# Optimization experiments

Hardware: AMD Instinct MI355X
Metric: run time of the kernel (lower is better)

The kernel has to match this reference:

```python
import math
import jax, jax.numpy as jnp
import numpy as np

NH, D, MULT, VOCAB, NLAYER = 4, 256, 128, 256, 2
N = MULT * D // NH  # 8192
EPS = 1e-5
THETA = 2.0 ** 16


def get_freqs(n):
    q = (jnp.arange(n, dtype=jnp.float32) // 2) * 2  # quantize(t, 2)
    return 1.0 / (THETA ** (q / n)) / (2 * math.pi)


def ln(x):
    # LayerNorm over last dim, no affine
    mu = jnp.mean(x, axis=-1, keepdims=True)
    var = jnp.mean((x - mu) ** 2, axis=-1, keepdims=True)
    return (x - mu) / jnp.sqrt(var + EPS)


def rope(phases, v):
    # phases: (T, N), v: (B, nh, T, N)
    ph = (phases % 1.0) * (2 * math.pi)
    c, s = jnp.cos(ph), jnp.sin(ph)
    v_rot = jnp.stack((-v[..., 1::2], v[..., ::2]), axis=-1).reshape(v.shape)
    return v * c + v_rot * s


def setup_inputs() -> dict:
    key = jax.random.key(0)
    ks = jax.random.split(key, 6)
    std = 0.02
    return {
        "idx": jax.random.randint(ks[0], (1, 2048), 0, VOCAB),
        "embed": jax.random.normal(ks[1], (VOCAB, D), jnp.float32) * std,
        "encoder": jax.random.normal(ks[2], (NH, D, N), jnp.float32) * std,
        "encoder_v": jax.random.normal(ks[3], (NH, D, N), jnp.float32) * std,
        "decoder": jax.random.normal(ks[4], (NH * N, D), jnp.float32) * std,
        "lm_head": jax.random.normal(ks[5], (D, VOCAB), jnp.float32) * std,
    }


def reference(idx, embed, encoder, encoder_v, decoder, lm_head):
    B, T = idx.shape
    freqs = get_freqs(N)  # (N,)
    phases = jnp.arange(T, dtype=jnp.float32)[:, None] * freqs[None, :]  # (T, N)
    # strictly-lower-triangular causal mask (tril diagonal=-1)
    t = jnp.arange(T)
    mask = (t[:, None] > t[None, :]).astype(jnp.float32)  # (T, T)

    x = ln(embed[idx][:, None])  # (B, 1, T, D)
    for _ in range(NLAYER):
        x_sparse = jax.nn.relu(jnp.einsum('bltd,hdn->bhtn', x, encoder))  # (B,nh,T,N)
        QR = rope(phases, x_sparse)
        scores = jnp.einsum('bhtn,bhsn->bhts', QR, QR) * mask  # (B,nh,T,T)
        yKV = ln(jnp.einsum('bhts,blsd->bhtd', scores, x))  # (B,nh,T,D)
        y_sparse = jax.nn.relu(jnp.einsum('bhtd,hdn->bhtn', yKV, encoder_v))
        xy = x_sparse * y_sparse  # (B,nh,T,N)
        xy = xy.transpose(0, 2, 1, 3).reshape(B, 1, T, NH * N)
        yMLP = xy @ decoder  # (B,1,T,D)
        x = ln(x + ln(yMLP))
    logits = x[:, 0] @ lm_head  # (B,T,vocab)
    return logits
```

## Files before the change

### kernel.cpp

```cpp
#include <hip/hip_runtime.h>
#include <hip/hip_bf16.h>
#include <math.h>

typedef unsigned short u16;
typedef unsigned int u32;
typedef __attribute__((ext_vector_type(8))) short short8;
typedef __attribute__((ext_vector_type(4))) float f32x4;

__device__ __forceinline__ u16 f2b(float f) {
  u32 u = __builtin_bit_cast(u32, f);
  u = (u + 0x7fffu + ((u >> 16) & 1u)) >> 16;
  return (u16)u;
}
__device__ __forceinline__ float b2f(u16 s) {
  return __builtin_bit_cast(float, (u32)s << 16);
}

__device__ __forceinline__ void ld_g2l(const u16* g, u16* l) {
  __builtin_amdgcn_global_load_lds(
      (const __attribute__((address_space(1))) unsigned int*)g,
      (__attribute__((address_space(3))) unsigned int*)l, 16, 0, 0);
}

__device__ __forceinline__ void gemm_core(
    const u16* __restrict__ A, const u16* __restrict__ B,
    int lda, int ldb, int Klen, int kb, int bm, int bn,
    u16* __restrict__ As, u16* __restrict__ Bs, f32x4 (&acc)[4][4])
{
  int tid = threadIdx.x;
  int w = tid >> 6, lane = tid & 63;
  int srow = (w << 4) + (lane >> 2);
  int scol = (lane & 3) << 3;
  const u16* ga0 = A + (long)(bm * 128 + srow) * lda + kb + scol;
  const u16* ga1 = ga0 + (long)64 * lda;
  const u16* gb0 = B + (long)(bn * 128 + srow) * ldb + kb + scol;
  const u16* gb1 = gb0 + (long)64 * ldb;
  u16* la0 = As + (w << 9);  u16* la1 = la0 + 2048;
  u16* lb0 = Bs + (w << 9);  u16* lb1 = lb0 + 2048;

  int wm = (w >> 1) << 6, wn = (w & 1) << 6;
  int lane15 = lane & 15, quad = lane >> 4;
  const u16* ar = As + (wm + lane15) * 32 + quad * 8;
  const u16* br = Bs + (wn + lane15) * 32 + quad * 8;

#pragma unroll
  for (int i = 0; i < 4; i++)
#pragma unroll
    for (int j = 0; j < 4; j++) { f32x4 z = {0.f, 0.f, 0.f, 0.f}; acc[i][j] = z; }

  for (int k = 0; k < Klen; k += 32) {
    ld_g2l(ga0 + k, la0);
    ld_g2l(ga1 + k, la1);
    ld_g2l(gb0 + k, lb0);
    ld_g2l(gb1 + k, lb1);
    __syncthreads();
    short8 af[4], bfr[4];
#pragma unroll
    for (int mt = 0; mt < 4; mt++) af[mt] = *(const short8*)(ar + mt * 16 * 32);
#pragma unroll
    for (int nt = 0; nt < 4; nt++) bfr[nt] = *(const short8*)(br + nt * 16 * 32);
#pragma unroll
    for (int mt = 0; mt < 4; mt++)
#pragma unroll
      for (int nt = 0; nt < 4; nt++)
        acc[mt][nt] = __builtin_amdgcn_mfma_f32_16x16x32_bf16(af[mt], bfr[nt], acc[mt][nt], 0, 0, 0);
    __syncthreads();
  }
}

__device__ __forceinline__ void rope_cs(int n, int t, float& c, float& s) {
  float f = exp2f((float)(-(n & ~1)) * (1.0f / 512.0f)) * 0.15915494f;
  float ph = (float)t * f;
  ph -= floorf(ph);
  __sincosf(ph * 6.2831853f, &s, &c);
}

template<int EPI>
__global__ __launch_bounds__(256, 2) void gemm_bt(
    const u16* __restrict__ A, const u16* __restrict__ B, void* __restrict__ C,
    int K, int lda, int ldb, int ldc, int nsplits, long aB, long bB, long cB,
    int tri)
{
  __shared__ __align__(16) u16 As[128 * 32];
  __shared__ __align__(16) u16 Bs[128 * 32];
  int bn = blockIdx.x, bm = blockIdx.y;
  int batch = blockIdx.z / nsplits, sp = blockIdx.z % nsplits;
  int Klen = K / nsplits, kb = sp * Klen;
  if (tri) {
    int kend = (bm + 1) * 128;
    if (kb >= kend) return;
    if (kb + Klen > kend) Klen = kend - kb;
  }

  f32x4 acc[4][4];
  gemm_core(A + (long)batch * aB, B + (long)batch * bB, lda, ldb, Klen, kb, bm, bn, As, Bs, acc);

  int lane = threadIdx.x & 63, w = threadIdx.x >> 6;
  int wm = (w >> 1) << 6, wn = (w & 1) << 6;
  int lane15 = lane & 15, quad = lane >> 4;

#pragma unroll
  for (int mt = 0; mt < 4; mt++)
#pragma unroll
    for (int nt = 0; nt < 4; nt++) {
      int gn = bn * 128 + wn + nt * 16 + lane15;
#pragma unroll
      for (int r = 0; r < 4; r++) {
        int gm = bm * 128 + wm + mt * 16 + quad * 4 + r;
        float v = acc[mt][nt][r];
        long ci = (long)batch * cB + (long)gm * ldc + gn;
        if (EPI == 0) {
          ((float*)C)[ci] = v;
        } else if (EPI == 1) {
          float rv = fmaxf(v, 0.f);
          float ro = __shfl_xor(rv, 1);
          float c, s; rope_cs(gn, gm, c, s);
          float out = (gn & 1) ? (rv * c + ro * s) : (rv * c - ro * s);
          ((u16*)C)[ci] = f2b(out);
        } else if (EPI == 3) {
          atomicAdd(&((float*)C)[ci], v);
        } else if (EPI == 4) {
          u16* Cp = (u16*)C;
          float q = b2f(Cp[ci]);
          float qo = __shfl_xor(q, 1);
          float c, s; rope_cs(gn, gm, c, s);
          float xs = (gn & 1) ? (q * c - qo * s) : (q * c + qo * s);
          Cp[ci] = f2b(fmaxf(v, 0.f) * xs);
        }
      }
    }
}

#define SC_BAR   __builtin_amdgcn_s_barrier()
#define SC_LGKM0 asm volatile("s_waitcnt lgkmcnt(0)" ::: "memory")
#define SC_LGKM8 asm volatile("s_waitcnt lgkmcnt(8)" ::: "memory")
#define SC_VMF   do { asm volatile("s_waitcnt vmcnt(4)" ::: "memory"); \
                      __builtin_amdgcn_sched_barrier(0); } while (0)
#define SC_P1    __builtin_amdgcn_s_setprio(1)
#define SC_P0    __builtin_amdgcn_s_setprio(0)

#define DSA(Ab, mh) { \
  _Pragma("unroll") for (int mt = 0; mt < 4; mt++) { \
    aA[mt][0] = *(const short8*)((Ab) + ((mh) * 64 + mt * 16) * 64 + koff0); \
    aA[mt][1] = *(const short8*)((Ab) + ((mh) * 64 + mt * 16) * 64 + koff1); } }

#define DSB(Bb, nh, dst) { \
  _Pragma("unroll") for (int nt = 0; nt < 2; nt++) { \
    dst[nt][0] = *(const short8*)((Bb) + ((nh) * 32 + nt * 16) * 64 + koff0); \
    dst[nt][1] = *(const short8*)((Bb) + ((nh) * 32 + nt * 16) * 64 + koff1); } }

#define MMA(MH, NH, BB) { \
  _Pragma("unroll") for (int mt = 0; mt < 4; mt++) \
  _Pragma("unroll") for (int nt = 0; nt < 2; nt++) { \
    acc[(MH)*4+mt][(NH)*2+nt] = __builtin_amdgcn_mfma_f32_16x16x32_bf16( \
        aA[mt][0], BB[nt][0], acc[(MH)*4+mt][(NH)*2+nt], 0, 0, 0); \
    acc[(MH)*4+mt][(NH)*2+nt] = __builtin_amdgcn_mfma_f32_16x16x32_bf16( \
        aA[mt][1], BB[nt][1], acc[(MH)*4+mt][(NH)*2+nt], 0, 0, 0); } }

__global__ __launch_bounds__(512, 1) void gemm_scores8(
    const u16* __restrict__ QR, u16* __restrict__ S, int T)
{
  __shared__ __align__(16) u16 Abuf[2][256 * 64];
  __shared__ __align__(16) u16 Bbuf[2][256 * 64];

  int q = blockIdx.x;
  int bm = (int)((sqrtf(8.f * (float)q + 1.f) - 1.f) * 0.5f);
  while ((bm + 1) * (bm + 2) / 2 <= q) bm++;
  while (bm * (bm + 1) / 2 > q) bm--;
  int bn = q - bm * (bm + 1) / 2;

  const u16* Q = QR + (long)blockIdx.z * (long)T * 8192;
  u16* Sb = S + (long)blockIdx.z * (long)T * T;

  int tid = threadIdx.x;
  int w = tid >> 6, lane = tid & 63;
  int wr = w >> 2, wc = w & 3;
  int lane15 = lane & 15, quad = lane >> 4;
  int swz = lane15 & 7;
  int koff0 = ((quad) ^ swz) << 3;
  int koff1 = ((4 + quad) ^ swz) << 3;

  const u16* gA = Q + (long)(bm * 256) * 8192;
  const u16* gB = Q + (long)(bn * 256) * 8192;

  const u16* A0 = &Abuf[0][(wr * 128 + lane15) * 64];
  const u16* A1 = &Abuf[1][(wr * 128 + lane15) * 64];
  const u16* B0 = &Bbuf[0][(wc * 64 + lane15) * 64];
  const u16* B1 = &Bbuf[1][(wc * 64 + lane15) * 64];

  int sr = lane >> 3, sc = lane & 7;
  long g_sk = (long)sr * 8192 + ((sc ^ sr) << 3);
  int l_base = (w * 16) * 64;
  long g_wrow = (long)(w * 16) * 8192;

  auto STG = [&](const u16* gHalfBase, u16* lHalfBase, int kt) {
    const u16* g = gHalfBase + g_wrow + g_sk + kt * 64;
    u16* l = lHalfBase + l_base;
    ld_g2l(g, l);
    ld_g2l(g + (long)8 * 8192, l + 8 * 64);
  };

  f32x4 acc[8][4];
#pragma unroll
  for (int i2 = 0; i2 < 8; i2++)
#pragma unroll
    for (int j = 0; j < 4; j++) { f32x4 z = {0.f, 0.f, 0.f, 0.f}; acc[i2][j] = z; }

  const long HSTEP = (long)128 * 8192;

  STG(gA, &Abuf[0][0], 0); STG(gA + HSTEP, &Abuf[0][128 * 64], 0);
  STG(gB, &Bbuf[0][0], 0); STG(gB + HSTEP, &Bbuf[0][128 * 64], 0);
  STG(gB, &Bbuf[1][0], 1); STG(gB + HSTEP, &Bbuf[1][128 * 64], 1);
  SC_VMF;
  SC_BAR;

  const int nkt = 8192 / 64;
  for (int i = 0; i < nkt / 2; i++) {
    int kt1 = 2 * i + 1;
    int kt2 = 2 * i + 2; if (kt2 > nkt - 1) kt2 = nkt - 1;
    int kt3 = 2 * i + 3; if (kt3 > nkt - 1) kt3 = nkt - 1;
    short8 aA[4][2], bb0[2][2], bb1[2][2];

    DSA(A0, 0); DSB(B0, 0, bb0);
    STG(gA, &Abuf[1][0], kt1);
    SC_LGKM8; SC_BAR; SC_LGKM0; SC_P1; MMA(0, 0, bb0); SC_P0; SC_BAR;
    DSB(B0, 1, bb1);
    STG(gA + HSTEP, &Abuf[1][128 * 64], kt1);
    SC_BAR; SC_LGKM0; SC_P1; MMA(0, 1, bb1); SC_P0; SC_BAR;
    DSA(A0, 1);
    STG(gB, &Bbuf[0][0], kt2);
    SC_BAR; SC_LGKM0; SC_P1; MMA(1, 1, bb1); SC_P0; SC_BAR;
    STG(gB + HSTEP, &Bbuf[0][128 * 64], kt2);
    SC_VMF; SC_BAR; SC_LGKM0; SC_P1; MMA(1, 0, bb0); SC_P0; SC_BAR;

    DSA(A1, 0); DSB(B1, 0, bb0);
    STG(gA, &Abuf[0][0], kt2);
    SC_LGKM8; SC_BAR; SC_LGKM0; SC_P1; MMA(0, 0, bb0); SC_P0; SC_BAR;
    DSB(B1, 1, bb1);
    STG(gA + HSTEP, &Abuf[0][128 * 64], kt2);
    SC_BAR; SC_LGKM0; SC_P1; MMA(0, 1, bb1); SC_P0; SC_BAR;
    DSA(A1, 1);
    STG(gB, &Bbuf[1][0], kt3);
    SC_BAR; SC_LGKM0; SC_P1; MMA(1, 1, bb1); SC_P0; SC_BAR;
    STG(gB + HSTEP, &Bbuf[1][128 * 64], kt3);
    SC_VMF; SC_BAR; SC_LGKM0; SC_P1; MMA(1, 0, bb0); SC_P0; SC_BAR;
  }

#pragma unroll
  for (int mt = 0; mt < 8; mt++)
#pragma unroll
    for (int nt = 0; nt < 4; nt++) {
      int gn = bn * 256 + wc * 64 + nt * 16 + lane15;
#pragma unroll
      for (int r = 0; r < 4; r++) {
        int gm = bm * 256 + wr * 128 + mt * 16 + quad * 4 + r;
        Sb[(long)gm * T + gn] = f2b(gm > gn ? acc[mt][nt][r] : 0.f);
      }
    }
}

__global__ __launch_bounds__(256) void trans_f32_bf16(
    const float* __restrict__ src, u16* __restrict__ dst, int R, int C)
{
  __shared__ float tile[32][33];
  long off = (long)blockIdx.z * R * C;
  const float* s = src + off;
  u16* d = dst + off;
  int lx = threadIdx.x & 31, ly = threadIdx.x >> 5;
  int c = blockIdx.x * 32 + lx;
#pragma unroll
  for (int p = 0; p < 32; p += 8)
    tile[ly + p][lx] = s[(long)(blockIdx.y * 32 + ly + p) * C + c];
  __syncthreads();
  int rr = blockIdx.y * 32 + lx;
#pragma unroll
  for (int p = 0; p < 32; p += 8)
    d[(long)(blockIdx.x * 32 + ly + p) * R + rr] = f2b(tile[lx][ly + p]);
}

__device__ __forceinline__ float block_sum(float v, float* red) {
#pragma unroll
  for (int o = 32; o > 0; o >>= 1) v += __shfl_down(v, o, 64);
  int lane = threadIdx.x & 63, wid = threadIdx.x >> 6;
  if (lane == 0) red[wid] = v;
  __syncthreads();
  float r = red[0] + red[1] + red[2] + red[3];
  __syncthreads();
  return r;
}

__global__ __launch_bounds__(256) void embed_ln(
    const int* __restrict__ idx, const float* __restrict__ embed,
    float* __restrict__ x, u16* __restrict__ xb, u16* __restrict__ xT, int T)
{
  __shared__ float red[4];
  int t = blockIdx.x, d = threadIdx.x;
  float v = embed[(long)idx[t] * 256 + d];
  float mu = block_sum(v, red) * (1.f / 256.f);
  float c = v - mu;
  float var = block_sum(c * c, red) * (1.f / 256.f);
  float o = c * rsqrtf(var + 1e-5f);
  x[(long)t * 256 + d] = o;
  xb[(long)t * 256 + d] = f2b(o);
  xT[(long)d * T + t] = f2b(o);
}

__global__ __launch_bounds__(256) void row_ln(
    const float* __restrict__ in, u16* __restrict__ out)
{
  __shared__ float red[4];
  long row = blockIdx.x;
  int d = threadIdx.x;
  float v = in[row * 256 + d];
  float mu = block_sum(v, red) * (1.f / 256.f);
  float c = v - mu;
  float var = block_sum(c * c, red) * (1.f / 256.f);
  out[row * 256 + d] = f2b(c * rsqrtf(var + 1e-5f));
}

__global__ __launch_bounds__(256) void resid_ln(
    const float* __restrict__ yMLP, float* __restrict__ x,
    u16* __restrict__ xb, u16* __restrict__ xT, int T)
{
  __shared__ float red[4];
  int t = blockIdx.x, d = threadIdx.x;
  float y = yMLP[(long)t * 256 + d];
  float mu1 = block_sum(y, red) * (1.f / 256.f);
  float c1 = y - mu1;
  float var1 = block_sum(c1 * c1, red) * (1.f / 256.f);
  float l1 = c1 * rsqrtf(var1 + 1e-5f);
  float v = x[(long)t * 256 + d] + l1;
  float mu2 = block_sum(v, red) * (1.f / 256.f);
  float c2 = v - mu2;
  float var2 = block_sum(c2 * c2, red) * (1.f / 256.f);
  float o = c2 * rsqrtf(var2 + 1e-5f);
  x[(long)t * 256 + d] = o;
  xb[(long)t * 256 + d] = f2b(o);
  xT[(long)d * T + t] = f2b(o);
}

extern "C" void kernel_launch(void* const* d_in, const int* in_sizes, int n_in,
                              void* d_out, int out_size, void* d_ws, size_t ws_size,
                              hipStream_t stream) {
  const int*   idx       = (const int*)d_in[0];
  const float* embed     = (const float*)d_in[1];
  const float* encoder   = (const float*)d_in[2];
  const float* encoder_v = (const float*)d_in[3];
  const float* decoder   = (const float*)d_in[4];
  const float* lm_head   = (const float*)d_in[5];
  const int T = in_sizes[0];
  const int D = 256, NH = 4, Nn = 8192, V = 256;

  char* ws = (char*)d_ws;
  size_t off = 0;
  auto alloc = [&](size_t bytes) -> void* {
    void* p = ws + off; off += (bytes + 255) & ~(size_t)255; return p;
  };
  float* x_f32   = (float*)alloc((size_t)T * D * 4);
  float* yMLP    = (float*)alloc((size_t)T * D * 4);
  float* yKV_f32 = (float*)alloc((size_t)NH * T * D * 4);
  u16* x_b    = (u16*)alloc((size_t)T * D * 2);
  u16* xT     = (u16*)alloc((size_t)T * D * 2);
  u16* yKV_b  = (u16*)alloc((size_t)NH * T * D * 2);
  u16* lmT    = (u16*)alloc((size_t)D * V * 2);
  u16* encT   = (u16*)alloc((size_t)NH * Nn * D * 2);
  u16* encvT  = (u16*)alloc((size_t)NH * Nn * D * 2);
  u16* decT   = (u16*)alloc((size_t)D * NH * Nn * 2);
  size_t per_head = ((size_t)T * T * 2 + 256) + ((size_t)T * Nn * 2 + 256);
  int HB = 4;
  while (HB > 1 && off + (size_t)HB * per_head > ws_size) HB >>= 1;
  u16* scores = (u16*)alloc((size_t)HB * T * T * 2);
  u16* QRxy   = (u16*)alloc((size_t)HB * T * Nn * 2);
  if (off > ws_size) return;

  trans_f32_bf16<<<dim3(Nn / 32, D / 32, NH), 256, 0, stream>>>(encoder, encT, D, Nn);
  trans_f32_bf16<<<dim3(Nn / 32, D / 32, NH), 256, 0, stream>>>(encoder_v, encvT, D, Nn);
  trans_f32_bf16<<<dim3(D / 32, (NH * Nn) / 32, 1), 256, 0, stream>>>(decoder, decT, NH * Nn, D);
  trans_f32_bf16<<<dim3(V / 32, D / 32, 1), 256, 0, stream>>>(lm_head, lmT, D, V);

  embed_ln<<<T, 256, 0, stream>>>(idx, embed, x_f32, x_b, xT, T);

  const int nbm = T / 256, ntri = nbm * (nbm + 1) / 2;

  for (int l = 0; l < 2; l++) {
    hipMemsetAsync(yMLP, 0, (size_t)T * D * 4, stream);
    for (int h0 = 0; h0 < NH; h0 += HB) {
      gemm_bt<1><<<dim3(Nn / 128, T / 128, HB), 256, 0, stream>>>(
          x_b, encT + (size_t)h0 * Nn * D, QRxy,
          D, D, D, Nn, 1, 0L, (long)Nn * D, (long)T * Nn, 0);
      gemm_scores8<<<dim3(ntri, 1, HB), 512, 0, stream>>>(QRxy, scores, T);
      hipMemsetAsync(yKV_f32, 0, (size_t)HB * T * D * 4, stream);
      gemm_bt<3><<<dim3(D / 128, T / 128, HB * 8), 256, 0, stream>>>(
          scores, xT, yKV_f32,
          T, T, T, D, 8, (long)T * T, 0L, (long)T * D, 1);
      row_ln<<<HB * T, 256, 0, stream>>>(yKV_f32, yKV_b);
      gemm_bt<4><<<dim3(Nn / 128, T / 128, HB), 256, 0, stream>>>(
          yKV_b, encvT + (size_t)h0 * Nn * D, QRxy,
          D, D, D, Nn, 1, (long)T * D, (long)Nn * D, (long)T * Nn, 0);
      gemm_bt<3><<<dim3(D / 128, T / 128, HB * 8), 256, 0, stream>>>(
          QRxy, decT + (size_t)h0 * Nn, yMLP,
          Nn, Nn, NH * Nn, D, 8, (long)T * Nn, (long)Nn, 0L, 0);
    }
    resid_ln<<<T, 256, 0, stream>>>(yMLP, x_f32, x_b, xT, T);
  }

  gemm_bt<0><<<dim3(V / 128, T / 128, 1), 256, 0, stream>>>(
      x_b, lmT, d_out, D, D, D, V, 1, 0L, 0L, 0L, 0);
}
```

Measured before the change: 1.214 ms.

## Generalize 256x256 eight-phase pipelined GEMM and use it for encoder and decoder GEMMs

Factors the eight-phase double-buffered 512-thread 256x256 MFMA loop from the scores kernel into a macro. It adds a templated general GEMM with the RoPE, relu-product and atomic epilogues. The encoder, encoder_v and decoder GEMMs switch from 128x128 256-thread tiles to this kernel, aiming for more reuse per block and better overlap of loads with MFMA. Grids shrink sharply (e.g. the decoder GEMM has only 1 N-tile), which risks lower occupancy or poor SM fill. K=256 also gives only 4 k-tiles, so the pipeline's prologue and epilogue dominate.

```diff
diff --git a/kernel.cpp b/kernel.cpp
--- a/kernel.cpp
+++ b/kernel.cpp
@@ -111,7 +111,227 @@
         long ci = (long)batch * cB + (long)gm * ldc + gn;
         if (EPI == 0) {
           ((float*)C)[ci] = v;
-        } else if (EPI == 1) {
+        } else if (EPI == 3) {
+          atomicAdd(&((float*)C)[ci], v);
+        }
+      }
+    }
+}
+
+#define SC_BAR   __builtin_amdgcn_s_barrier()
+#define SC_LGKM0 asm volatile("s_waitcnt lgkmcnt(0)" ::: "memory")
+#define SC_LGKM8 asm volatile("s_waitcnt lgkmcnt(8)" ::: "memory")
+#define SC_VMF   do { asm volatile("s_waitcnt vmcnt(4)" ::: "memory"); \
+                      __builtin_amdgcn_sched_barrier(0); } while (0)
+#define SC_P1    __builtin_amdgcn_s_setprio(1)
+#define SC_P0    __builtin_amdgcn_s_setprio(0)
+
+#define DSA(Ab, mh) { \
+  _Pragma("unroll") for (int mt = 0; mt < 4; mt++) { \
+    aA[mt][0] = *(const short8*)((Ab) + ((mh) * 64 + mt * 16) * 64 + koff0); \
+    aA[mt][1] = *(const short8*)((Ab) + ((mh) * 64 + mt * 16) * 64 + koff1); } }
+
+#define DSB(Bb, nh, dst) { \
+  _Pragma("unroll") for (int nt = 0; nt < 2; nt++) { \
+    dst[nt][0] = *(const short8*)((Bb) + ((nh) * 32 + nt * 16) * 64 + koff0); \
+    dst[nt][1] = *(const short8*)((Bb) + ((nh) * 32 + nt * 16) * 64 + koff1); } }
+
+#define MMA(MH, NH, BB) { \
+  _Pragma("unroll") for (int mt = 0; mt < 4; mt++) \
+  _Pragma("unroll") for (int nt = 0; nt < 2; nt++) { \
+    acc[(MH)*4+mt][(NH)*2+nt] = __builtin_amdgcn_mfma_f32_16x16x32_bf16( \
+        aA[mt][0], BB[nt][0], acc[(MH)*4+mt][(NH)*2+nt], 0, 0, 0); \
+    acc[(MH)*4+mt][(NH)*2+nt] = __builtin_amdgcn_mfma_f32_16x16x32_bf16( \
+        aA[mt][1], BB[nt][1], acc[(MH)*4+mt][(NH)*2+nt], 0, 0, 0); } }
+
+#define EIGHT_PHASE_LOOP(STGA, STGB) \
+  for (int i = 0; i < nkt / 2; i++) { \
+    int kt1 = 2 * i + 1; \
+    int kt2 = 2 * i + 2; if (kt2 > nkt - 1) kt2 = nkt - 1; \
+    int kt3 = 2 * i + 3; if (kt3 > nkt - 1) kt3 = nkt - 1; \
+    short8 aA[4][2], bb0[2][2], bb1[2][2]; \
+     \
+    DSA(A0, 0); DSB(B0, 0, bb0); \
+    STGA(gA, &Abuf[1][0], kt1); \
+    SC_LGKM8; SC_BAR; SC_LGKM0; SC_P1; MMA(0, 0, bb0); SC_P0; SC_BAR; \
+     \
+    DSB(B0, 1, bb1); \
+    STGA(gA + HSTEPA, &Abuf[1][128 * 64], kt1); \
+    SC_BAR; SC_LGKM0; SC_P1; MMA(0, 1, bb1); SC_P0; SC_BAR; \
+     \
+    DSA(A0, 1); \
+    STGB(gB, &Bbuf[0][0], kt2); \
+    SC_BAR; SC_LGKM0; SC_P1; MMA(1, 1, bb1); SC_P0; SC_BAR; \
+     \
+    STGB(gB + HSTEPB, &Bbuf[0][128 * 64], kt2); \
+    SC_VMF; SC_BAR; SC_LGKM0; SC_P1; MMA(1, 0, bb0); SC_P0; SC_BAR; \
+     \
+    DSA(A1, 0); DSB(B1, 0, bb0); \
+    STGA(gA, &Abuf[0][0], kt2); \
+    SC_LGKM8; SC_BAR; SC_LGKM0; SC_P1; MMA(0, 0, bb0); SC_P0; SC_BAR; \
+     \
+    DSB(B1, 1, bb1); \
+    STGA(gA + HSTEPA, &Abuf[0][128 * 64], kt2); \
+    SC_BAR; SC_LGKM0; SC_P1; MMA(0, 1, bb1); SC_P0; SC_BAR; \
+     \
+    DSA(A1, 1); \
+    STGB(gB, &Bbuf[1][0], kt3); \
+    SC_BAR; SC_LGKM0; SC_P1; MMA(1, 1, bb1); SC_P0; SC_BAR; \
+     \
+    STGB(gB + HSTEPB, &Bbuf[1][128 * 64], kt3); \
+    SC_VMF; SC_BAR; SC_LGKM0; SC_P1; MMA(1, 0, bb0); SC_P0; SC_BAR; \
+  }
+
+__global__ __launch_bounds__(512, 1) void gemm_scores8(
+    const u16* __restrict__ QR, u16* __restrict__ S, int T)
+{
+  __shared__ __align__(16) u16 Abuf[2][256 * 64];
+  __shared__ __align__(16) u16 Bbuf[2][256 * 64];
+
+  int q = blockIdx.x;
+  int bm = (int)((sqrtf(8.f * (float)q + 1.f) - 1.f) * 0.5f);
+  while ((bm + 1) * (bm + 2) / 2 <= q) bm++;
+  while (bm * (bm + 1) / 2 > q) bm--;
+  int bn = q - bm * (bm + 1) / 2;
+
+  const u16* Q = QR + (long)blockIdx.z * (long)T * 8192;
+  u16* Sb = S + (long)blockIdx.z * (long)T * T;
+
+  int tid = threadIdx.x;
+  int w = tid >> 6, lane = tid & 63;
+  int wr = w >> 2, wc = w & 3;
+  int lane15 = lane & 15, quad = lane >> 4;
+  int swz = lane15 & 7;
+  int koff0 = ((quad) ^ swz) << 3;
+  int koff1 = ((4 + quad) ^ swz) << 3;
+
+  const u16* gA = Q + (long)(bm * 256) * 8192;
+  const u16* gB = Q + (long)(bn * 256) * 8192;
+
+  const u16* A0 = &Abuf[0][(wr * 128 + lane15) * 64];
+  const u16* A1 = &Abuf[1][(wr * 128 + lane15) * 64];
+  const u16* B0 = &Bbuf[0][(wc * 64 + lane15) * 64];
+  const u16* B1 = &Bbuf[1][(wc * 64 + lane15) * 64];
+
+  int sr = lane >> 3, sc = lane & 7;
+  long g_sk = (long)sr * 8192 + ((sc ^ sr) << 3);
+  int l_base = (w * 16) * 64;
+  long g_wrow = (long)(w * 16) * 8192;
+
+  auto STG = [&](const u16* gHalfBase, u16* lHalfBase, int kt) {
+    const u16* g = gHalfBase + g_wrow + g_sk + kt * 64;
+    u16* l = lHalfBase + l_base;
+    ld_g2l(g, l);
+    ld_g2l(g + (long)8 * 8192, l + 8 * 64);
+  };
+
+  f32x4 acc[8][4];
+#pragma unroll
+  for (int i2 = 0; i2 < 8; i2++)
+#pragma unroll
+    for (int j = 0; j < 4; j++) { f32x4 z = {0.f, 0.f, 0.f, 0.f}; acc[i2][j] = z; }
+
+  const long HSTEPA = (long)128 * 8192;
+  const long HSTEPB = HSTEPA;
+
+  STG(gA, &Abuf[0][0], 0); STG(gA + HSTEPA, &Abuf[0][128 * 64], 0);
+  STG(gB, &Bbuf[0][0], 0); STG(gB + HSTEPB, &Bbuf[0][128 * 64], 0);
+  STG(gB, &Bbuf[1][0], 1); STG(gB + HSTEPB, &Bbuf[1][128 * 64], 1);
+  SC_VMF;
+  SC_BAR;
+
+  const int nkt = 8192 / 64;
+  EIGHT_PHASE_LOOP(STG, STG)
+
+#pragma unroll
+  for (int mt = 0; mt < 8; mt++)
+#pragma unroll
+    for (int nt = 0; nt < 4; nt++) {
+      int gn = bn * 256 + wc * 64 + nt * 16 + lane15;
+#pragma unroll
+      for (int r = 0; r < 4; r++) {
+        int gm = bm * 256 + wr * 128 + mt * 16 + quad * 4 + r;
+        Sb[(long)gm * T + gn] = f2b(gm > gn ? acc[mt][nt][r] : 0.f);
+      }
+    }
+}
+
+template<int EPI>
+__global__ __launch_bounds__(512, 1) void gemm256_8ph(
+    const u16* __restrict__ A, const u16* __restrict__ B, void* __restrict__ C,
+    int K, int lda, int ldb, int ldc, int nsplits, long aB, long bB, long cB)
+{
+  __shared__ __align__(16) u16 Abuf[2][256 * 64];
+  __shared__ __align__(16) u16 Bbuf[2][256 * 64];
+
+  int bn = blockIdx.x, bm = blockIdx.y;
+  int batch = blockIdx.z / nsplits, sp = blockIdx.z % nsplits;
+  int Klen = K / nsplits, kb = sp * Klen;
+  int nkt = Klen >> 6;
+
+  int tid = threadIdx.x;
+  int w = tid >> 6, lane = tid & 63;
+  int wr = w >> 2, wc = w & 3;
+  int lane15 = lane & 15, quad = lane >> 4;
+  int swz = lane15 & 7;
+  int koff0 = ((quad) ^ swz) << 3;
+  int koff1 = ((4 + quad) ^ swz) << 3;
+
+  const u16* gA = A + (long)batch * aB + (long)(bm * 256) * lda + kb;
+  const u16* gB = B + (long)batch * bB + (long)(bn * 256) * ldb + kb;
+
+  const u16* A0 = &Abuf[0][(wr * 128 + lane15) * 64];
+  const u16* A1 = &Abuf[1][(wr * 128 + lane15) * 64];
+  const u16* B0 = &Bbuf[0][(wc * 64 + lane15) * 64];
+  const u16* B1 = &Bbuf[1][(wc * 64 + lane15) * 64];
+
+  int sr = lane >> 3, sc = lane & 7;
+  int l_base = (w * 16) * 64;
+  long g_skA = (long)sr * lda + ((sc ^ sr) << 3);
+  long g_skB = (long)sr * ldb + ((sc ^ sr) << 3);
+  long g_wrowA = (long)(w * 16) * lda;
+  long g_wrowB = (long)(w * 16) * ldb;
+  const long HSTEPA = (long)128 * lda;
+  const long HSTEPB = (long)128 * ldb;
+
+  auto STGA = [&](const u16* gHalfBase, u16* lHalfBase, int kt) {
+    const u16* g = gHalfBase + g_wrowA + g_skA + kt * 64;
+    u16* l = lHalfBase + l_base;
+    ld_g2l(g, l);
+    ld_g2l(g + (long)8 * lda, l + 8 * 64);
+  };
+  auto STGB = [&](const u16* gHalfBase, u16* lHalfBase, int kt) {
+    const u16* g = gHalfBase + g_wrowB + g_skB + kt * 64;
+    u16* l = lHalfBase + l_base;
+    ld_g2l(g, l);
+    ld_g2l(g + (long)8 * ldb, l + 8 * 64);
+  };
+
+  f32x4 acc[8][4];
+#pragma unroll
+  for (int i2 = 0; i2 < 8; i2++)
+#pragma unroll
+    for (int j = 0; j < 4; j++) { f32x4 z = {0.f, 0.f, 0.f, 0.f}; acc[i2][j] = z; }
+
+  STGA(gA, &Abuf[0][0], 0); STGA(gA + HSTEPA, &Abuf[0][128 * 64], 0);
+  STGB(gB, &Bbuf[0][0], 0); STGB(gB + HSTEPB, &Bbuf[0][128 * 64], 0);
+  STGB(gB, &Bbuf[1][0], 1); STGB(gB + HSTEPB, &Bbuf[1][128 * 64], 1);
+  SC_VMF;
+  SC_BAR;
+
+  EIGHT_PHASE_LOOP(STGA, STGB)
+
+#pragma unroll
+  for (int mt = 0; mt < 8; mt++)
+#pragma unroll
+    for (int nt = 0; nt < 4; nt++) {
+      int gn = bn * 256 + wc * 64 + nt * 16 + lane15;
+#pragma unroll
+      for (int r = 0; r < 4; r++) {
+        int gm = bm * 256 + wr * 128 + mt * 16 + quad * 4 + r;
+        float v = acc[mt][nt][r];
+        long ci = (long)batch * cB + (long)gm * ldc + gn;
+        if (EPI == 1) {
           float rv = fmaxf(v, 0.f);
           float ro = __shfl_xor(rv, 1);
           float c, s; rope_cs(gn, gm, c, s);
@@ -121,140 +341,12 @@
           atomicAdd(&((float*)C)[ci], v);
         } else if (EPI == 4) {
           u16* Cp = (u16*)C;
-          float q = b2f(Cp[ci]);
-          float qo = __shfl_xor(q, 1);
+          float qv = b2f(Cp[ci]);
+          float qo = __shfl_xor(qv, 1);
           float c, s; rope_cs(gn, gm, c, s);
-          float xs = (gn & 1) ? (q * c - qo * s) : (q * c + qo * s);
+          float xs = (gn & 1) ? (qv * c - qo * s) : (qv * c + qo * s);
           Cp[ci] = f2b(fmaxf(v, 0.f) * xs);
         }
-      }
-    }
-}
-
-#define SC_BAR   __builtin_amdgcn_s_barrier()
-#define SC_LGKM0 asm volatile("s_waitcnt lgkmcnt(0)" ::: "memory")
-#define SC_LGKM8 asm volatile("s_waitcnt lgkmcnt(8)" ::: "memory")
-#define SC_VMF   do { asm volatile("s_waitcnt vmcnt(4)" ::: "memory"); \
-                      __builtin_amdgcn_sched_barrier(0); } while (0)
-#define SC_P1    __builtin_amdgcn_s_setprio(1)
-#define SC_P0    __builtin_amdgcn_s_setprio(0)
-
-#define DSA(Ab, mh) { \
-  _Pragma("unroll") for (int mt = 0; mt < 4; mt++) { \
-    aA[mt][0] = *(const short8*)((Ab) + ((mh) * 64 + mt * 16) * 64 + koff0); \
-    aA[mt][1] = *(const short8*)((Ab) + ((mh) * 64 + mt * 16) * 64 + koff1); } }
-
-#define DSB(Bb, nh, dst) { \
-  _Pragma("unroll") for (int nt = 0; nt < 2; nt++) { \
-    dst[nt][0] = *(const short8*)((Bb) + ((nh) * 32 + nt * 16) * 64 + koff0); \
-    dst[nt][1] = *(const short8*)((Bb) + ((nh) * 32 + nt * 16) * 64 + koff1); } }
-
-#define MMA(MH, NH, BB) { \
-  _Pragma("unroll") for (int mt = 0; mt < 4; mt++) \
-  _Pragma("unroll") for (int nt = 0; nt < 2; nt++) { \
-    acc[(MH)*4+mt][(NH)*2+nt] = __builtin_amdgcn_mfma_f32_16x16x32_bf16( \
-        aA[mt][0], BB[nt][0], acc[(MH)*4+mt][(NH)*2+nt], 0, 0, 0); \
-    acc[(MH)*4+mt][(NH)*2+nt] = __builtin_amdgcn_mfma_f32_16x16x32_bf16( \
-        aA[mt][1], BB[nt][1], acc[(MH)*4+mt][(NH)*2+nt], 0, 0, 0); } }
-
-__global__ __launch_bounds__(512, 1) void gemm_scores8(
-    const u16* __restrict__ QR, u16* __restrict__ S, int T)
-{
-  __shared__ __align__(16) u16 Abuf[2][256 * 64];
-  __shared__ __align__(16) u16 Bbuf[2][256 * 64];
-
-  int q = blockIdx.x;
-  int bm = (int)((sqrtf(8.f * (float)q + 1.f) - 1.f) * 0.5f);
-  while ((bm + 1) * (bm + 2) / 2 <= q) bm++;
-  while (bm * (bm + 1) / 2 > q) bm--;
-  int bn = q - bm * (bm + 1) / 2;
-
-  const u16* Q = QR + (long)blockIdx.z * (long)T * 8192;
-  u16* Sb = S + (long)blockIdx.z * (long)T * T;
-
-  int tid = threadIdx.x;
-  int w = tid >> 6, lane = tid & 63;
-  int wr = w >> 2, wc = w & 3;
-  int lane15 = lane & 15, quad = lane >> 4;
-  int swz = lane15 & 7;
-  int koff0 = ((quad) ^ swz) << 3;
-  int koff1 = ((4 + quad) ^ swz) << 3;
-
-  const u16* gA = Q + (long)(bm * 256) * 8192;
-  const u16* gB = Q + (long)(bn * 256) * 8192;
-
-  const u16* A0 = &Abuf[0][(wr * 128 + lane15) * 64];
-  const u16* A1 = &Abuf[1][(wr * 128 + lane15) * 64];
-  const u16* B0 = &Bbuf[0][(wc * 64 + lane15) * 64];
-  const u16* B1 = &Bbuf[1][(wc * 64 + lane15) * 64];
-
-  int sr = lane >> 3, sc = lane & 7;
-  long g_sk = (long)sr * 8192 + ((sc ^ sr) << 3);
-  int l_base = (w * 16) * 64;
-  long g_wrow = (long)(w * 16) * 8192;
-
-  auto STG = [&](const u16* gHalfBase, u16* lHalfBase, int kt) {
-    const u16* g = gHalfBase + g_wrow + g_sk + kt * 64;
-    u16* l = lHalfBase + l_base;
-    ld_g2l(g, l);
-    ld_g2l(g + (long)8 * 8192, l + 8 * 64);
-  };
-
-  f32x4 acc[8][4];
-#pragma unroll
-  for (int i2 = 0; i2 < 8; i2++)
-#pragma unroll
-    for (int j = 0; j < 4; j++) { f32x4 z = {0.f, 0.f, 0.f, 0.f}; acc[i2][j] = z; }
-
-  const long HSTEP = (long)128 * 8192;
-
-  STG(gA, &Abuf[0][0], 0); STG(gA + HSTEP, &Abuf[0][128 * 64], 0);
-  STG(gB, &Bbuf[0][0], 0); STG(gB + HSTEP, &Bbuf[0][128 * 64], 0);
-  STG(gB, &Bbuf[1][0], 1); STG(gB + HSTEP, &Bbuf[1][128 * 64], 1);
-  SC_VMF;
-  SC_BAR;
-
-  const int nkt = 8192 / 64;
-  for (int i = 0; i < nkt / 2; i++) {
-    int kt1 = 2 * i + 1;
-    int kt2 = 2 * i + 2; if (kt2 > nkt - 1) kt2 = nkt - 1;
-    int kt3 = 2 * i + 3; if (kt3 > nkt - 1) kt3 = nkt - 1;
-    short8 aA[4][2], bb0[2][2], bb1[2][2];
-
-    DSA(A0, 0); DSB(B0, 0, bb0);
-    STG(gA, &Abuf[1][0], kt1);
-    SC_LGKM8; SC_BAR; SC_LGKM0; SC_P1; MMA(0, 0, bb0); SC_P0; SC_BAR;
-    DSB(B0, 1, bb1);
-    STG(gA + HSTEP, &Abuf[1][128 * 64], kt1);
-    SC_BAR; SC_LGKM0; SC_P1; MMA(0, 1, bb1); SC_P0; SC_BAR;
-    DSA(A0, 1);
-    STG(gB, &Bbuf[0][0], kt2);
-    SC_BAR; SC_LGKM0; SC_P1; MMA(1, 1, bb1); SC_P0; SC_BAR;
-    STG(gB + HSTEP, &Bbuf[0][128 * 64], kt2);
-    SC_VMF; SC_BAR; SC_LGKM0; SC_P1; MMA(1, 0, bb0); SC_P0; SC_BAR;
-
-    DSA(A1, 0); DSB(B1, 0, bb0);
-    STG(gA, &Abuf[0][0], kt2);
-    SC_LGKM8; SC_BAR; SC_LGKM0; SC_P1; MMA(0, 0, bb0); SC_P0; SC_BAR;
-    DSB(B1, 1, bb1);
-    STG(gA + HSTEP, &Abuf[0][128 * 64], kt2);
-    SC_BAR; SC_LGKM0; SC_P1; MMA(0, 1, bb1); SC_P0; SC_BAR;
-    DSA(A1, 1);
-    STG(gB, &Bbuf[1][0], kt3);
-    SC_BAR; SC_LGKM0; SC_P1; MMA(1, 1, bb1); SC_P0; SC_BAR;
-    STG(gB + HSTEP, &Bbuf[1][128 * 64], kt3);
-    SC_VMF; SC_BAR; SC_LGKM0; SC_P1; MMA(1, 0, bb0); SC_P0; SC_BAR;
-  }
-
-#pragma unroll
-  for (int mt = 0; mt < 8; mt++)
-#pragma unroll
-    for (int nt = 0; nt < 4; nt++) {
-      int gn = bn * 256 + wc * 64 + nt * 16 + lane15;
-#pragma unroll
-      for (int r = 0; r < 4; r++) {
-        int gm = bm * 256 + wr * 128 + mt * 16 + quad * 4 + r;
-        Sb[(long)gm * T + gn] = f2b(gm > gn ? acc[mt][nt][r] : 0.f);
       }
     }
 }
@@ -385,21 +477,21 @@
   for (int l = 0; l < 2; l++) {
     hipMemsetAsync(yMLP, 0, (size_t)T * D * 4, stream);
     for (int h0 = 0; h0 < NH; h0 += HB) {
-      gemm_bt<1><<<dim3(Nn / 128, T / 128, HB), 256, 0, stream>>>(
+      gemm256_8ph<1><<<dim3(Nn / 256, T / 256, HB), 512, 0, stream>>>(
           x_b, encT + (size_t)h0 * Nn * D, QRxy,
-          D, D, D, Nn, 1, 0L, (long)Nn * D, (long)T * Nn, 0);
+          D, D, D, Nn, 1, 0L, (long)Nn * D, (long)T * Nn);
       gemm_scores8<<<dim3(ntri, 1, HB), 512, 0, stream>>>(QRxy, scores, T);
       hipMemsetAsync(yKV_f32, 0, (size_t)HB * T * D * 4, stream);
       gemm_bt<3><<<dim3(D / 128, T / 128, HB * 8), 256, 0, stream>>>(
           scores, xT, yKV_f32,
           T, T, T, D, 8, (long)T * T, 0L, (long)T * D, 1);
       row_ln<<<HB * T, 256, 0, stream>>>(yKV_f32, yKV_b);
-      gemm_bt<4><<<dim3(Nn / 128, T / 128, HB), 256, 0, stream>>>(
+      gemm256_8ph<4><<<dim3(Nn / 256, T / 256, HB), 512, 0, stream>>>(
           yKV_b, encvT + (size_t)h0 * Nn * D, QRxy,
-          D, D, D, Nn, 1, (long)T * D, (long)Nn * D, (long)T * Nn, 0);
-      gemm_bt<3><<<dim3(D / 128, T / 128, HB * 8), 256, 0, stream>>>(
+          D, D, D, Nn, 1, (long)T * D, (long)Nn * D, (long)T * Nn);
+      gemm256_8ph<3><<<dim3(1, T / 256, HB * 8), 512, 0, stream>>>(
           QRxy, decT + (size_t)h0 * Nn, yMLP,
-          Nn, Nn, NH * Nn, D, 8, (long)T * Nn, (long)Nn, 0L, 0);
+          Nn, Nn, NH * Nn, D, 8, (long)T * Nn, (long)Nn, 0L);
     }
     resid_ln<<<T, 256, 0, stream>>>(yMLP, x_f32, x_b, xT, T);
   }
```

Result: slower. 1.303 ms (+7.4%).
